# Kernel optimization log

Hardware: AMD Instinct MI355X
Metric: run time of the kernel (lower is better)

Reference implementation:

```python
import jax, jax.numpy as jnp
import numpy as np

N_HEAD = 16
ROPE_BASE = 10000.0


def setup_inputs() -> dict:
    key = jax.random.key(0)
    k1, k2, k3 = jax.random.split(key, 3)
    B, T, C = 2, 2048, 2048
    x = jax.random.normal(k1, (B, T, C), dtype=jnp.float32)
    # 0.02 init scale keeps attention logits in a sane range
    w_qkv = jax.random.normal(k2, (3 * C, C), dtype=jnp.float32) * 0.02
    w_proj = jax.random.normal(k3, (C, C), dtype=jnp.float32) * 0.02
    return {"x": x, "w_qkv": w_qkv, "w_proj": w_proj}


def _apply_rope(t, cos, sin):
    # t: [B, T, H, hd]; cos/sin: [T, hd//2]
    B, T, H, hd = t.shape
    ts = t.reshape(B, T, H, hd // 2, 2)
    x0, x1 = ts[..., 0], ts[..., 1]
    c = cos[None, :, None, :]
    s = sin[None, :, None, :]
    out = jnp.stack([x0 * c - x1 * s, x1 * c + x0 * s], axis=-1)
    return out.reshape(B, T, H, hd)


def reference(x, w_qkv, w_proj):
    B, T, C = x.shape
    H = N_HEAD
    hd = C // H

    qkv = x @ w_qkv.T                       # [B, T, 3C]
    q, k, v = jnp.split(qkv, 3, axis=2)
    q = q.reshape(B, T, H, hd)
    k = k.reshape(B, T, H, hd)              # present kv: pre-RoPE k, [B,T,H,hd]
    v = v.reshape(B, T, H, hd).transpose(0, 2, 1, 3)  # [B,H,T,hd]

    # RoPE cache (positions = arange(T) since past_key_value is None)
    theta = 1.0 / (ROPE_BASE ** (jnp.arange(0, hd, 2, dtype=jnp.float32) / hd))
    ang = jnp.arange(T, dtype=jnp.float32)[:, None] * theta[None, :]  # [T, hd//2]
    cos, sin = jnp.cos(ang), jnp.sin(ang)

    qr = _apply_rope(q, cos, sin).transpose(0, 2, 1, 3)  # [B,H,T,hd]
    kr = _apply_rope(k, cos, sin).transpose(0, 2, 1, 3)  # [B,H,T,hd]

    scale = 1.0 / jnp.sqrt(jnp.asarray(hd, dtype=qr.dtype))
    scores = jnp.einsum('bhqd,bhkd->bhqk', qr, kr) * scale  # [B,H,T,T]
    attn = jax.nn.softmax(scores, axis=-1)
    o = jnp.einsum('bhqk,bhkd->bhqd', attn, v)              # [B,H,T,hd]
    y = o.transpose(0, 2, 1, 3).reshape(B, T, C) @ w_proj.T
    return (y, k, v)
```

## Files before the change

### kernel.cpp

```cpp
#include <hip/hip_runtime.h>
#include <math.h>


typedef __bf16 bf16_t;
typedef __bf16 bf16x8 __attribute__((ext_vector_type(8)));
typedef __bf16 bf16x4v __attribute__((ext_vector_type(4)));
typedef float  f32x4  __attribute__((ext_vector_type(4)));

#define B_  2
#define T_  2048
#define C_  2048
#define SLICE_ ((size_t)B_ * T_ * C_)

__device__ __forceinline__ void glds16(const void* g, void* l) {
  __builtin_amdgcn_global_load_lds(
      (__attribute__((address_space(1))) void*)(void*)(const_cast<void*>(g)),
      (__attribute__((address_space(3))) void*)(l), 16, 0, 0);
}

__global__ __launch_bounds__(256) void k_cvt(const float4* __restrict__ in,
                                             bf16x4v* __restrict__ out, int n4) {
  int i = blockIdx.x * 256 + threadIdx.x;
  if (i < n4) {
    float4 v = in[i];
    bf16x4v o;
    o[0] = (bf16_t)v.x; o[1] = (bf16_t)v.y; o[2] = (bf16_t)v.z; o[3] = (bf16_t)v.w;
    out[i] = o;
  }
}

__global__ __launch_bounds__(256) void k_tab(float2* __restrict__ tab) {
  int i = blockIdx.x * 256 + threadIdx.x;
  int t = i >> 6, j = i & 63;
  float thf = (float)pow(10000.0, -(double)(2 * j) / 128.0);
  float angf = (float)t * thf;
  double a = (double)angf;
  tab[i] = make_float2((float)cos(a), (float)sin(a));
}


struct FragA { bf16x8 v[4][2]; };
struct FragB { bf16x8 v[2][2]; };

__device__ __forceinline__ void stage_half(const bf16_t* __restrict__ g, int k0,
                                           bf16_t* l, int H, int tid) {
  const int wv = tid >> 6;
#pragma unroll
  for (int s = 0; s < 2; ++s) {
    int ci = s * 512 + tid;
    int row = ci >> 3;
    glds16(g + (size_t)(H * 128 + row) * 2048 + k0 + (((ci & 7) ^ (row & 7)) << 3),
           l + H * 8192 + (size_t)(s * 512 + wv * 64) * 8);
  }
}

__device__ __forceinline__ void load_afrags(const bf16_t* buf, int ha, int wm,
                                            int l16, int q4, FragA& fa) {
#pragma unroll
  for (int mf = 0; mf < 4; ++mf) {
    const bf16_t* rp = buf + (ha * 128 + wm * 64 + mf * 16 + l16) * 64;
#pragma unroll
    for (int ks = 0; ks < 2; ++ks)
      fa.v[mf][ks] = *(const bf16x8*)(rp + ((((ks << 2) | q4) ^ (l16 & 7)) << 3));
  }
}

__device__ __forceinline__ void load_bfrags(const bf16_t* buf, int hb, int wn,
                                            int l16, int q4, FragB& fb) {
#pragma unroll
  for (int nf = 0; nf < 2; ++nf) {
    const bf16_t* rp = buf + (hb * 128 + wn * 32 + nf * 16 + l16) * 64;
#pragma unroll
    for (int ks = 0; ks < 2; ++ks)
      fb.v[nf][ks] = *(const bf16x8*)(rp + ((((ks << 2) | q4) ^ (l16 & 7)) << 3));
  }
}

template <int HA, int HB>
__device__ __forceinline__ void phase_mfma(const FragA& fa, const FragB& fb,
                                           f32x4 (&acc)[2][4][2][2]) {
  __builtin_amdgcn_s_setprio(1);
#pragma unroll
  for (int ks = 0; ks < 2; ++ks)
#pragma unroll
    for (int mf = 0; mf < 4; ++mf)
#pragma unroll
      for (int nf = 0; nf < 2; ++nf)
        acc[HA][mf][HB][nf] = __builtin_amdgcn_mfma_f32_16x16x32_bf16(
            fa.v[mf][ks], fb.v[nf][ks], acc[HA][mf][HB][nf], 0, 0, 0);
  __builtin_amdgcn_s_setprio(0);
}

#define BARRIER() asm volatile("s_barrier" ::: "memory")
#define VMCNT4()  asm volatile("s_waitcnt vmcnt(4)" ::: "memory")

__global__ __launch_bounds__(512, 1) void k_qkv(
    const bf16_t* __restrict__ X, const bf16_t* __restrict__ W,
    const float2* __restrict__ tab,
    bf16_t* __restrict__ qb, bf16_t* __restrict__ kb, bf16_t* __restrict__ vtb,
    float* __restrict__ kout, float* __restrict__ vout) {
  const int K = 2048;
  extern __shared__ char smem_raw[];
  bf16_t* sm = (bf16_t*)smem_raw;
  bf16_t* AE = sm;
  bf16_t* AO = sm + 16384;
  bf16_t* BE = sm + 32768;
  bf16_t* BO = sm + 49152;

  const int tid = threadIdx.x;
  const int lane = tid & 63, wv = tid >> 6;
  const int wm = wv >> 2, wn = wv & 3;
  const int q4 = lane >> 4, l16 = lane & 15;

  const int bid = blockIdx.x;
  const int swz = (bid & 7) * 48 + (bid >> 3);
  const int m0 = (swz & 15) * 256;
  const int n0 = (swz >> 4) * 256;

  const bf16_t* Ab = X + (size_t)m0 * K;
  const bf16_t* Wb = W + (size_t)n0 * K;

  f32x4 acc[2][4][2][2];
  {
    f32x4 zero4 = {0.f, 0.f, 0.f, 0.f};
#pragma unroll
    for (int ha = 0; ha < 2; ++ha)
#pragma unroll
      for (int mf = 0; mf < 4; ++mf)
#pragma unroll
        for (int hb = 0; hb < 2; ++hb)
#pragma unroll
          for (int nf = 0; nf < 2; ++nf) acc[ha][mf][hb][nf] = zero4;
  }

  stage_half(Ab, 0, AE, 0, tid);
  stage_half(Wb, 0, BE, 0, tid);
  stage_half(Wb, 0, BE, 1, tid);
  stage_half(Ab, 0, AE, 1, tid);
  stage_half(Ab, 64, AO, 0, tid);
  stage_half(Wb, 64, BO, 1, tid);
  VMCNT4();
  BARRIER();

  for (int t = 0; t < 16; ++t) {
    const int kO  = t * 128 + 64;
    const int kE2 = (t * 128 + 128) & 2047;
    const int kO2 = (t * 128 + 192) & 2047;

    FragA fa; FragB fb;
    load_afrags(AE, 0, wm, l16, q4, fa);
    load_bfrags(BE, 0, wn, l16, q4, fb);
    stage_half(Wb, kO, BO, 0, tid);
    stage_half(Ab, kO, AO, 1, tid);
    BARRIER();
    phase_mfma<0, 0>(fa, fb, acc);
    BARRIER();
    load_bfrags(BE, 1, wn, l16, q4, fb);
    BARRIER();
    phase_mfma<0, 1>(fa, fb, acc);
    BARRIER();
    load_afrags(AE, 1, wm, l16, q4, fa);
    stage_half(Ab, kE2, AE, 0, tid);
    BARRIER();
    phase_mfma<1, 1>(fa, fb, acc);
    BARRIER();
    load_bfrags(BE, 0, wn, l16, q4, fb);
    stage_half(Wb, kE2, BE, 1, tid);
    VMCNT4();
    BARRIER();
    phase_mfma<1, 0>(fa, fb, acc);
    BARRIER();
    load_afrags(AO, 0, wm, l16, q4, fa);
    load_bfrags(BO, 0, wn, l16, q4, fb);
    stage_half(Wb, kE2, BE, 0, tid);
    stage_half(Ab, kE2, AE, 1, tid);
    BARRIER();
    phase_mfma<0, 0>(fa, fb, acc);
    BARRIER();
    load_bfrags(BO, 1, wn, l16, q4, fb);
    BARRIER();
    phase_mfma<0, 1>(fa, fb, acc);
    BARRIER();
    load_afrags(AO, 1, wm, l16, q4, fa);
    stage_half(Ab, kO2, AO, 0, tid);
    BARRIER();
    phase_mfma<1, 1>(fa, fb, acc);
    BARRIER();
    load_bfrags(BO, 0, wn, l16, q4, fb);
    stage_half(Wb, kO2, BO, 1, tid);
    VMCNT4();
    BARRIER();
    phase_mfma<1, 0>(fa, fb, acc);
    BARRIER();
  }

  __syncthreads();

  const int sec = n0 >> 11;
  const int t0 = m0 & 2047, bb = m0 >> 11, h0 = (n0 & 2047) >> 7;

  if (sec < 2) {
#pragma unroll
    for (int ha = 0; ha < 2; ++ha) {
      if (ha) __syncthreads();
#pragma unroll
      for (int mf = 0; mf < 4; ++mf)
#pragma unroll
        for (int hb = 0; hb < 2; ++hb)
#pragma unroll
          for (int nf = 0; nf < 2; ++nf)
#pragma unroll
            for (int r = 0; r < 4; ++r) {
              int mlr = wm * 64 + mf * 16 + q4 * 4 + r;
              int d2  = hb * 128 + wn * 32 + nf * 16 + l16;
              int d   = d2 & 127;
              float val = acc[ha][mf][hb][nf][r];
              float partner = __shfl_xor(val, 1);
              float2 cs = tab[(t0 + ha * 128 + mlr) * 64 + (d >> 1)];
              float rv = (d & 1) ? (val * cs.x + partner * cs.y)
                                 : (val * cs.x - partner * cs.y);
              if (sec == 0) rv *= 0.08838834764831845f;
              else kout[(size_t)(m0 + ha * 128 + mlr) * 2048 +
                        (h0 + hb) * 128 + d] = val;
              sm[mlr * 264 + d2] = (bf16_t)rv;
            }
      __syncthreads();
      bf16_t* dst = (sec == 0 ? qb : kb);
#pragma unroll
      for (int i = 0; i < 8; ++i) {
        int ci = i * 512 + tid;
        int mlr = ci >> 5, cc = (ci & 31) * 8;
        int hs = cc >> 7, d = cc & 127;
        *(bf16x8*)(dst +
                   ((size_t)(bb * 16 + h0 + hs) * 2048 + t0 + ha * 128 + mlr) * 128 +
                   d) = *(const bf16x8*)&sm[mlr * 264 + cc];
      }
    }
  } else {
#pragma unroll
    for (int hb = 0; hb < 2; ++hb) {
      if (hb) __syncthreads();
#pragma unroll
      for (int ha = 0; ha < 2; ++ha)
#pragma unroll
        for (int mf = 0; mf < 4; ++mf)
#pragma unroll
          for (int nf = 0; nf < 2; ++nf)
#pragma unroll
            for (int r = 0; r < 4; ++r) {
              int ml = ha * 128 + wm * 64 + mf * 16 + q4 * 4 + r;
              int d2 = hb * 128 + wn * 32 + nf * 16 + l16;
              int d  = d2 & 127;
              float val = acc[ha][mf][hb][nf][r];
              vout[((size_t)(bb * 16 + h0 + hb) * 2048 + t0 + ml) * 128 + d] = val;
              sm[d * 264 + ml] = (bf16_t)val;
            }
      __syncthreads();
#pragma unroll
      for (int i = 0; i < 8; ++i) {
        int ci = i * 512 + tid;
        int dr = ci >> 5, cc = (ci & 31) * 8;
        *(bf16x8*)(vtb +
                   ((size_t)((bb * 16 + h0 + hb) * 128 + dr)) * 2048 + t0 + cc) =
            *(const bf16x8*)&sm[dr * 264 + cc];
      }
    }
  }
}

__global__ __launch_bounds__(256, 2) void k_attn(
    const bf16_t* __restrict__ qb, const bf16_t* __restrict__ kb,
    const bf16_t* __restrict__ vtb, bf16_t* __restrict__ ob) {
  __shared__ alignas(16) bf16_t Ps[128 * 80];
  __shared__ alignas(16) bf16_t Ks[64 * 128];
  __shared__ alignas(16) bf16_t Vts[128 * 64];

  const int tid = threadIdx.x;
  const int lane = tid & 63, wv = tid >> 6;
  const int q4 = lane >> 4, l16 = lane & 15;
  const int bh = blockIdx.x >> 4;
  const int q0 = (blockIdx.x & 15) * 128;

  const bf16_t* Qg = qb + (size_t)bh * T_ * 128 + (size_t)q0 * 128;
  const bf16_t* Kg = kb + (size_t)bh * T_ * 128;
  const bf16_t* Vg = vtb + (size_t)bh * 128 * T_;

  bf16x8 qa[2][4];
#pragma unroll
  for (int mf = 0; mf < 2; ++mf)
#pragma unroll
    for (int kf = 0; kf < 4; ++kf)
      qa[mf][kf] = *(const bf16x8*)(Qg + (size_t)(wv * 32 + mf * 16 + l16) * 128 +
                                    kf * 32 + q4 * 8);

  f32x4 zero4 = {0.f, 0.f, 0.f, 0.f};
  float lrow[2][4];
  f32x4 oacc[2][8];
#pragma unroll
  for (int mf = 0; mf < 2; ++mf) {
#pragma unroll
    for (int r = 0; r < 4; ++r) lrow[mf][r] = 0.f;
#pragma unroll
    for (int nf = 0; nf < 8; ++nf) oacc[mf][nf] = zero4;
  }

  for (int key0 = 0; key0 < T_; key0 += 64) {
    __syncthreads();
#pragma unroll
    for (int i = 0; i < 4; ++i) {
      int ci = i * 256 + tid;
      glds16(Kg + (size_t)(key0 + (ci >> 4)) * 128 +
                 (((ci & 15) ^ ((ci >> 4) & 7)) << 3),
             &Ks[(i * 256 + wv * 64) * 8]);
    }
#pragma unroll
    for (int i = 0; i < 4; ++i) {
      int ci = i * 256 + tid;
      glds16(Vg + (size_t)(ci >> 3) * T_ + key0 +
                 (((ci & 7) ^ ((ci >> 3) & 7)) << 3),
             &Vts[(i * 256 + wv * 64) * 8]);
    }
    __syncthreads();

    f32x4 sacc[2][4];
#pragma unroll
    for (int mf = 0; mf < 2; ++mf)
#pragma unroll
      for (int nf = 0; nf < 4; ++nf) sacc[mf][nf] = zero4;
#pragma unroll
    for (int kf = 0; kf < 4; ++kf) {
      bf16x8 bfrag[4];
#pragma unroll
      for (int nf = 0; nf < 4; ++nf)
        bfrag[nf] = *(const bf16x8*)&Ks[(nf * 16 + l16) * 128 +
                                        ((((kf << 2) | q4) ^ (l16 & 7)) << 3)];
#pragma unroll
      for (int mf = 0; mf < 2; ++mf)
#pragma unroll
        for (int nf = 0; nf < 4; ++nf)
          sacc[mf][nf] = __builtin_amdgcn_mfma_f32_16x16x32_bf16(
              qa[mf][kf], bfrag[nf], sacc[mf][nf], 0, 0, 0);
    }

#pragma unroll
    for (int mf = 0; mf < 2; ++mf) {
#pragma unroll
      for (int r = 0; r < 4; ++r) {
        float p0 = __expf(sacc[mf][0][r]);
        float p1 = __expf(sacc[mf][1][r]);
        float p2 = __expf(sacc[mf][2][r]);
        float p3 = __expf(sacc[mf][3][r]);
        int prow = wv * 32 + mf * 16 + q4 * 4 + r;
        Ps[prow * 80 + 0 + l16]  = (bf16_t)p0;
        Ps[prow * 80 + 16 + l16] = (bf16_t)p1;
        Ps[prow * 80 + 32 + l16] = (bf16_t)p2;
        Ps[prow * 80 + 48 + l16] = (bf16_t)p3;
        lrow[mf][r] += (p0 + p1) + (p2 + p3);
      }
    }

#pragma unroll
    for (int kf2 = 0; kf2 < 2; ++kf2) {
      bf16x8 pa[2], vb[8];
#pragma unroll
      for (int mf = 0; mf < 2; ++mf)
        pa[mf] = *(const bf16x8*)&Ps[(wv * 32 + mf * 16 + l16) * 80 +
                                     kf2 * 32 + q4 * 8];
#pragma unroll
      for (int nf = 0; nf < 8; ++nf)
        vb[nf] = *(const bf16x8*)&Vts[(nf * 16 + l16) * 64 +
                                      ((((kf2 << 2) | q4) ^ (l16 & 7)) << 3)];
#pragma unroll
      for (int mf = 0; mf < 2; ++mf)
#pragma unroll
        for (int nf = 0; nf < 8; ++nf)
          oacc[mf][nf] = __builtin_amdgcn_mfma_f32_16x16x32_bf16(
              pa[mf], vb[nf], oacc[mf][nf], 0, 0, 0);
    }
  }

  const int b = bh >> 4, h = bh & 15;
#pragma unroll
  for (int mf = 0; mf < 2; ++mf) {
#pragma unroll
    for (int r = 0; r < 4; ++r) {
      float l = lrow[mf][r];
      l += __shfl_xor(l, 1);
      l += __shfl_xor(l, 2);
      l += __shfl_xor(l, 4);
      l += __shfl_xor(l, 8);
      float inv = 1.f / l;
      int t = q0 + wv * 32 + mf * 16 + q4 * 4 + r;
      size_t base = ((size_t)b * 2048 + t) * 2048 + h * 128;
#pragma unroll
      for (int nf = 0; nf < 8; ++nf)
        ob[base + nf * 16 + l16] = (bf16_t)(oacc[mf][nf][r] * inv);
    }
  }
}

__global__ __launch_bounds__(256, 2) void k_proj(
    const bf16_t* __restrict__ O, const bf16_t* __restrict__ Wp,
    float* __restrict__ Y) {
  const int K = 2048;
  __shared__ alignas(16) bf16_t As[128 * 64];
  __shared__ alignas(16) bf16_t Bs[128 * 64];
  const int tid = threadIdx.x;
  const int lane = tid & 63, wv = tid >> 6;
  const int wm = wv >> 1, wn = wv & 1;
  const int q4 = lane >> 4, l16 = lane & 15;
  const int m0 = blockIdx.x * 128, n0 = blockIdx.y * 128;

  const bf16_t* Ab = O + (size_t)m0 * K;
  const bf16_t* Wb = Wp + (size_t)n0 * K;

  f32x4 zero4 = {0.f, 0.f, 0.f, 0.f};
  f32x4 acc[4][4];
#pragma unroll
  for (int i = 0; i < 4; ++i)
#pragma unroll
    for (int j = 0; j < 4; ++j) acc[i][j] = zero4;

  for (int k0 = 0; k0 < K; k0 += 64) {
    __syncthreads();
#pragma unroll
    for (int i = 0; i < 4; ++i) {
      int ci = i * 256 + tid;
      glds16(Ab + (size_t)(ci >> 3) * K + k0 + (((ci & 7) ^ ((ci >> 3) & 7)) << 3),
             &As[(i * 256 + wv * 64) * 8]);
    }
#pragma unroll
    for (int i = 0; i < 4; ++i) {
      int ci = i * 256 + tid;
      glds16(Wb + (size_t)(ci >> 3) * K + k0 + (((ci & 7) ^ ((ci >> 3) & 7)) << 3),
             &Bs[(i * 256 + wv * 64) * 8]);
    }
    __syncthreads();
#pragma unroll
    for (int kk = 0; kk < 2; ++kk) {
      bf16x8 afrag[4], bfrag[4];
#pragma unroll
      for (int mf = 0; mf < 4; ++mf)
        afrag[mf] = *(const bf16x8*)&As[(wm * 64 + mf * 16 + l16) * 64 +
                                        ((((kk << 2) | q4) ^ (l16 & 7)) << 3)];
#pragma unroll
      for (int nf = 0; nf < 4; ++nf)
        bfrag[nf] = *(const bf16x8*)&Bs[(wn * 64 + nf * 16 + l16) * 64 +
                                        ((((kk << 2) | q4) ^ (l16 & 7)) << 3)];
#pragma unroll
      for (int mf = 0; mf < 4; ++mf)
#pragma unroll
        for (int nf = 0; nf < 4; ++nf)
          acc[mf][nf] = __builtin_amdgcn_mfma_f32_16x16x32_bf16(
              afrag[mf], bfrag[nf], acc[mf][nf], 0, 0, 0);
    }
  }
#pragma unroll
  for (int mf = 0; mf < 4; ++mf)
#pragma unroll
    for (int nf = 0; nf < 4; ++nf)
#pragma unroll
      for (int r = 0; r < 4; ++r) {
        int m = m0 + wm * 64 + mf * 16 + q4 * 4 + r;
        int n = n0 + wn * 64 + nf * 16 + l16;
        Y[(size_t)m * 2048 + n] = acc[mf][nf][r];
      }
}

extern "C" void kernel_launch(void* const* d_in, const int* in_sizes, int n_in,
                              void* d_out, int out_size, void* d_ws, size_t ws_size,
                              hipStream_t stream) {
  const float* x = (const float*)d_in[0];
  const float* wqkv = (const float*)d_in[1];
  const float* wproj = (const float*)d_in[2];

  float* y = (float*)d_out;
  float* kout = y + SLICE_;
  float* vout = y + 2 * SLICE_;

  char* w = (char*)d_ws;
  bf16_t* xb = (bf16_t*)w;      w += SLICE_ * 2;
  bf16_t* wqkvb = (bf16_t*)w;   w += (size_t)12582912 * 2;
  bf16_t* wprojb = (bf16_t*)w;  w += (size_t)4194304 * 2;
  bf16_t* qb = (bf16_t*)w;      w += SLICE_ * 2;
  bf16_t* kb = (bf16_t*)w;      w += SLICE_ * 2;
  bf16_t* vtb = (bf16_t*)w;     w += SLICE_ * 2;
  bf16_t* ob = (bf16_t*)w;      w += SLICE_ * 2;
  float2* tab = (float2*)w;     w += (size_t)131072 * 8;
  (void)ws_size; (void)in_sizes; (void)n_in; (void)out_size;

  static int smem_set = 0;
  if (!smem_set) {
    hipFuncSetAttribute((const void*)k_qkv,
                        hipFuncAttributeMaxDynamicSharedMemorySize, 131072);
    smem_set = 1;
  }

  k_cvt<<<8192, 256, 0, stream>>>((const float4*)x, (bf16x4v*)xb, 2097152);
  k_cvt<<<12288, 256, 0, stream>>>((const float4*)wqkv, (bf16x4v*)wqkvb, 3145728);
  k_cvt<<<4096, 256, 0, stream>>>((const float4*)wproj, (bf16x4v*)wprojb, 1048576);
  k_tab<<<512, 256, 0, stream>>>(tab);

  k_qkv<<<384, 512, 131072, stream>>>(xb, wqkvb, tab, qb, kb, vtb, kout, vout);
  k_attn<<<512, 256, 0, stream>>>(qb, kb, vtb, ob);
  dim3 gp(32, 16);
  k_proj<<<gp, 256, 0, stream>>>(ob, wprojb, y);
}
```

Measured before the change: 431.5 us.

## Rewrite QKV GEMM main loop with inline-asm LDS reads and fewer barriers

```diff
diff --git a/kernel.cpp b/kernel.cpp
--- a/kernel.cpp
+++ b/kernel.cpp
@@ -16,6 +16,10 @@
   __builtin_amdgcn_global_load_lds(
       (__attribute__((address_space(1))) void*)(void*)(const_cast<void*>(g)),
       (__attribute__((address_space(3))) void*)(l), 16, 0, 0);
+}
+
+__device__ __forceinline__ unsigned ldsaddr(const void* p) {
+  return (unsigned)(size_t)(__attribute__((address_space(3))) const void*)(p);
 }
 
 __global__ __launch_bounds__(256) void k_cvt(const float4* __restrict__ in,
@@ -54,31 +58,24 @@
   }
 }
 
-__device__ __forceinline__ void load_afrags(const bf16_t* buf, int ha, int wm,
-                                            int l16, int q4, FragA& fa) {
-#pragma unroll
-  for (int mf = 0; mf < 4; ++mf) {
-    const bf16_t* rp = buf + (ha * 128 + wm * 64 + mf * 16 + l16) * 64;
-#pragma unroll
-    for (int ks = 0; ks < 2; ++ks)
-      fa.v[mf][ks] = *(const bf16x8*)(rp + ((((ks << 2) | q4) ^ (l16 & 7)) << 3));
-  }
-}
-
-__device__ __forceinline__ void load_bfrags(const bf16_t* buf, int hb, int wn,
-                                            int l16, int q4, FragB& fb) {
-#pragma unroll
-  for (int nf = 0; nf < 2; ++nf) {
-    const bf16_t* rp = buf + (hb * 128 + wn * 32 + nf * 16 + l16) * 64;
-#pragma unroll
-    for (int ks = 0; ks < 2; ++ks)
-      fb.v[nf][ks] = *(const bf16x8*)(rp + ((((ks << 2) | q4) ^ (l16 & 7)) << 3));
-  }
-}
+#define LDSR(r, a, OFF) \
+  asm volatile("ds_read_b128 %0, %1 offset:" #OFF : "=v"(r) : "v"(a))
+#define RD_A8(F, a0, a1, B0, B1, B2, B3) do { \
+  LDSR((F).v[0][0], a0, B0); LDSR((F).v[0][1], a1, B0); \
+  LDSR((F).v[1][0], a0, B1); LDSR((F).v[1][1], a1, B1); \
+  LDSR((F).v[2][0], a0, B2); LDSR((F).v[2][1], a1, B2); \
+  LDSR((F).v[3][0], a0, B3); LDSR((F).v[3][1], a1, B3); } while (0)
+#define RD_B4(F, b0, b1, C0, C1) do { \
+  LDSR((F).v[0][0], b0, C0); LDSR((F).v[0][1], b1, C0); \
+  LDSR((F).v[1][0], b0, C1); LDSR((F).v[1][1], b1, C1); } while (0)
+#define LGKM(n) asm volatile("s_waitcnt lgkmcnt(" #n ")")
+#define SCHED0() __builtin_amdgcn_sched_barrier(0)
+#define BARRIER() asm volatile("s_barrier" ::: "memory")
+#define VMCNT(n) asm volatile("s_waitcnt vmcnt(" #n ")" ::: "memory")
 
 template <int HA, int HB>
-__device__ __forceinline__ void phase_mfma(const FragA& fa, const FragB& fb,
-                                           f32x4 (&acc)[2][4][2][2]) {
+__device__ __forceinline__ void mfma_q(const FragA& fa, const FragB& fb,
+                                       f32x4 (&acc)[2][4][2][2]) {
   __builtin_amdgcn_s_setprio(1);
 #pragma unroll
   for (int ks = 0; ks < 2; ++ks)
@@ -90,9 +87,6 @@
             fa.v[mf][ks], fb.v[nf][ks], acc[HA][mf][HB][nf], 0, 0, 0);
   __builtin_amdgcn_s_setprio(0);
 }
-
-#define BARRIER() asm volatile("s_barrier" ::: "memory")
-#define VMCNT4()  asm volatile("s_waitcnt vmcnt(4)" ::: "memory")
 
 __global__ __launch_bounds__(512, 1) void k_qkv(
     const bf16_t* __restrict__ X, const bf16_t* __restrict__ W,
@@ -120,6 +114,16 @@
   const bf16_t* Ab = X + (size_t)m0 * K;
   const bf16_t* Wb = W + (size_t)n0 * K;
 
+  const int c0 = (q4 ^ (l16 & 7)) << 4;
+  const int c1 = ((4 | q4) ^ (l16 & 7)) << 4;
+  const unsigned lb = ldsaddr(sm);
+  const unsigned aAE0 = lb + (wm * 64 + l16) * 128 + c0;
+  const unsigned aAE1 = lb + (wm * 64 + l16) * 128 + c1;
+  const unsigned aAO0 = aAE0 + 32768, aAO1 = aAE1 + 32768;
+  const unsigned aBE0 = lb + 65536 + (wn * 32 + l16) * 128 + c0;
+  const unsigned aBE1 = lb + 65536 + (wn * 32 + l16) * 128 + c1;
+  const unsigned aBO0 = aBE0 + 32768, aBO1 = aBE1 + 32768;
+
   f32x4 acc[2][4][2][2];
   {
     f32x4 zero4 = {0.f, 0.f, 0.f, 0.f};
@@ -133,67 +137,71 @@
           for (int nf = 0; nf < 2; ++nf) acc[ha][mf][hb][nf] = zero4;
   }
 
+  FragA faA, faB;
+  FragB fb0, fb1, fb2, fb3;
+
   stage_half(Ab, 0, AE, 0, tid);
+  stage_half(Ab, 0, AE, 1, tid);
   stage_half(Wb, 0, BE, 0, tid);
   stage_half(Wb, 0, BE, 1, tid);
-  stage_half(Ab, 0, AE, 1, tid);
   stage_half(Ab, 64, AO, 0, tid);
+  stage_half(Ab, 64, AO, 1, tid);
+  stage_half(Wb, 64, BO, 0, tid);
   stage_half(Wb, 64, BO, 1, tid);
-  VMCNT4();
+  VMCNT(8);
   BARRIER();
-
+  RD_A8(faA, aAE0, aAE1, 0, 2048, 4096, 6144);
+  RD_B4(fb0, aBE0, aBE1, 0, 2048);
+  RD_B4(fb1, aBE0, aBE1, 16384, 18432);
+
+#pragma unroll 1
   for (int t = 0; t < 16; ++t) {
-    const int kO  = t * 128 + 64;
     const int kE2 = (t * 128 + 128) & 2047;
     const int kO2 = (t * 128 + 192) & 2047;
 
-    FragA fa; FragB fb;
-    load_afrags(AE, 0, wm, l16, q4, fa);
-    load_bfrags(BE, 0, wn, l16, q4, fb);
-    stage_half(Wb, kO, BO, 0, tid);
-    stage_half(Ab, kO, AO, 1, tid);
-    BARRIER();
-    phase_mfma<0, 0>(fa, fb, acc);
-    BARRIER();
-    load_bfrags(BE, 1, wn, l16, q4, fb);
-    BARRIER();
-    phase_mfma<0, 1>(fa, fb, acc);
-    BARRIER();
-    load_afrags(AE, 1, wm, l16, q4, fa);
+    LGKM(4); SCHED0();
+    mfma_q<0, 0>(faA, fb0, acc);
+    BARRIER();
+    RD_A8(faB, aAE0, aAE1, 16384, 18432, 20480, 22528);
     stage_half(Ab, kE2, AE, 0, tid);
-    BARRIER();
-    phase_mfma<1, 1>(fa, fb, acc);
-    BARRIER();
-    load_bfrags(BE, 0, wn, l16, q4, fb);
+    stage_half(Wb, kE2, BE, 0, tid);
+    LGKM(8); SCHED0();
+    mfma_q<0, 1>(faA, fb1, acc);
+    VMCNT(4);
+    BARRIER();
+    RD_A8(faA, aAO0, aAO1, 0, 2048, 4096, 6144);
+    RD_B4(fb2, aBO0, aBO1, 0, 2048);
     stage_half(Wb, kE2, BE, 1, tid);
-    VMCNT4();
-    BARRIER();
-    phase_mfma<1, 0>(fa, fb, acc);
-    BARRIER();
-    load_afrags(AO, 0, wm, l16, q4, fa);
-    load_bfrags(BO, 0, wn, l16, q4, fb);
-    stage_half(Wb, kE2, BE, 0, tid);
+    LGKM(12); SCHED0();
+    mfma_q<1, 1>(faB, fb1, acc);
+    BARRIER();
+    RD_B4(fb3, aBO0, aBO1, 16384, 18432);
     stage_half(Ab, kE2, AE, 1, tid);
-    BARRIER();
-    phase_mfma<0, 0>(fa, fb, acc);
-    BARRIER();
-    load_bfrags(BO, 1, wn, l16, q4, fb);
-    BARRIER();
-    phase_mfma<0, 1>(fa, fb, acc);
-    BARRIER();
-    load_afrags(AO, 1, wm, l16, q4, fa);
+    mfma_q<1, 0>(faB, fb0, acc);
+    BARRIER();
+    RD_A8(faB, aAO0, aAO1, 16384, 18432, 20480, 22528);
+    LGKM(12); SCHED0();
+    mfma_q<0, 0>(faA, fb2, acc);
+    BARRIER();
     stage_half(Ab, kO2, AO, 0, tid);
-    BARRIER();
-    phase_mfma<1, 1>(fa, fb, acc);
-    BARRIER();
-    load_bfrags(BO, 0, wn, l16, q4, fb);
+    stage_half(Wb, kO2, BO, 0, tid);
+    LGKM(8); SCHED0();
+    mfma_q<0, 1>(faA, fb3, acc);
+    VMCNT(4);
+    BARRIER();
+    RD_A8(faA, aAE0, aAE1, 0, 2048, 4096, 6144);
+    RD_B4(fb0, aBE0, aBE1, 0, 2048);
     stage_half(Wb, kO2, BO, 1, tid);
-    VMCNT4();
-    BARRIER();
-    phase_mfma<1, 0>(fa, fb, acc);
-    BARRIER();
-  }
-
+    LGKM(12); SCHED0();
+    mfma_q<1, 1>(faB, fb3, acc);
+    BARRIER();
+    RD_B4(fb1, aBE0, aBE1, 16384, 18432);
+    stage_half(Ab, kO2, AO, 1, tid);
+    mfma_q<1, 0>(faB, fb2, acc);
+    BARRIER();
+  }
+
+  asm volatile("s_waitcnt vmcnt(0) lgkmcnt(0)" ::: "memory");
   __syncthreads();
 
   const int sec = n0 >> 11;
```

Result: slower. 660.6 us (+53.1%).
